# Optimization experiments

Measured on AMD Instinct MI355X. Metric: run time of the kernel, lower is better.

The kernel has to match this reference:

```python
import jax, jax.numpy as jnp
import numpy as np

B, T, E, H = 4, 2048, 1024, 16
D = E // H  # head dim = 64


def setup_inputs() -> dict:
    key = jax.random.key(0)
    k1, k2, k3 = jax.random.split(key, 3)
    g = jax.random.normal(k1, (B, T, E), dtype=jnp.float32)
    W_lift = jax.random.normal(k2, (2 * E, E), dtype=jnp.float32) * (1.0 / np.sqrt(E))
    W_proj = jax.random.normal(k3, (H, H), dtype=jnp.float32) * (1.0 / np.sqrt(H))
    return {"g": g, "W_lift": W_lift, "W_proj": W_proj}


def reference(g, W_lift, W_proj):
    b, t, e = g.shape
    h, d = H, e // H
    # lift: Linear(E, 2E, bias=False) -> split into q, k
    qk = jnp.einsum('bte,fe->btf', g, W_lift)  # (B, T, 2E)
    q, k = qk[..., :e], qk[..., e:]
    q = q.reshape(b, t, h, d).transpose(0, 2, 1, 3)  # (B, H, T, D)
    k = k.reshape(b, t, h, d).transpose(0, 2, 1, 3)  # (B, H, T, D)
    # unscaled causal scores
    a = jnp.einsum('bhqd,bhkd->bhqk', q, k)  # (B, H, T, T)
    causal = jnp.tril(jnp.ones((t, t), dtype=bool))
    a = jnp.where(causal[None, None], a, -jnp.inf)
    # masked logsumexp over key dim -> (B, H, T)
    lse = jax.scipy.special.logsumexp(a, axis=-1)
    out = lse.transpose(0, 2, 1)  # (B, T, H)
    out = jnp.einsum('bth,gh->btg', out, W_proj)  # proj Linear(H, H)
    out = out.sum(axis=2)  # (B, T)
    return out.reshape(-1, out.shape[-1])
```

## Files before the change

kernel.cpp:

```cpp
#include <hip/hip_runtime.h>
#include <hip/hip_bf16.h>

#define B_ 4
#define T_ 2048
#define E_ 1024
#define H_ 16
#define D_ 64
#define Mtot 8192
#define N2 2048
#define K_ 1024
#define PS_ (B_ * H_ * T_)
#define NKT 16
#define LOG2E 1.4426950408889634f

typedef __attribute__((ext_vector_type(8))) short short8;
typedef __attribute__((ext_vector_type(4))) float f32x4;
using bf16 = __hip_bfloat16;

__device__ __forceinline__ void async_copy16(const void* g, void* l) {
  __builtin_amdgcn_global_load_lds(
      (const __attribute__((address_space(1))) unsigned int*)g,
      (__attribute__((address_space(3))) unsigned int*)l, 16, 0, 0);
}

__global__ void cast_f32_to_bf16(const float* __restrict__ in, ushort* __restrict__ out, int n4) {
  int stride = gridDim.x * blockDim.x;
  for (int i = blockIdx.x * blockDim.x + threadIdx.x; i < n4; i += stride) {
    float4 v = reinterpret_cast<const float4*>(in)[i];
    bf16 a = __float2bfloat16(v.x), b = __float2bfloat16(v.y);
    bf16 c = __float2bfloat16(v.z), d = __float2bfloat16(v.w);
    ushort4 o = make_ushort4(*(ushort*)&a, *(ushort*)&b, *(ushort*)&c, *(ushort*)&d);
    reinterpret_cast<ushort4*>(out)[i] = o;
  }
}

#define MFMA_BF16(a, b, c) __builtin_amdgcn_mfma_f32_16x16x32_bf16(a, b, c, 0, 0, 0)

__launch_bounds__(512, 2)
__global__ void lift_gemm(const bf16* __restrict__ A, const bf16* __restrict__ Bm,
                          bf16* __restrict__ qh, bf16* __restrict__ kh) {
  __shared__ __align__(16) char sL[8][16384];
  const int bid = blockIdx.x;
  const int swz = ((bid & 7) << 5) | (bid >> 3);
  const int m0 = (swz >> 3) * 256;
  const int n0 = (swz & 7) * 256;
  const int tid = threadIdx.x;
  const int lane = tid & 63, w = tid >> 6;
  const int wm = w >> 2, wn = w & 3;
  const int lr = lane & 15, lg = lane >> 4;

  f32x4 acc[8][4];
#pragma unroll
  for (int i = 0; i < 8; ++i)
#pragma unroll
    for (int j = 0; j < 4; ++j) acc[i][j] = (f32x4)(0.0f);

  auto stage_half = [&](int slot, const bf16* gsrc, int Rbase, int kcol) {
#pragma unroll
    for (int it = 0; it < 2; ++it) {
      const int o = ((it * 512 + tid) << 4);
      const int lin = o ^ (((o >> 7) & 7) << 4);
      const int r = lin >> 7, cb = lin & 127;
      async_copy16((const char*)gsrc + ((size_t)(Rbase + r) * K_ + kcol) * 2 + cb,
                   &sL[slot][o]);
    }
  };
  auto rd = [&](int slot, int row, int khalf) -> short8 {
    int off = (row << 7) + (khalf << 6) + (lg << 4);
    off ^= (row & 7) << 4;
    return *(const short8*)&sL[slot][off];
  };

  stage_half(0, A, m0, 0);
  stage_half(1, A, m0 + 128, 0);
  stage_half(2, Bm, n0, 0);
  stage_half(3, Bm, n0 + 128, 0);

  for (int kt = 0; kt < NKT; ++kt) {
    const int cb = (kt & 1) << 2;
    const int nb = cb ^ 4;
    const int kcol = (kt + 1) * 64;
    const int aslot = cb + wm;
    const int bslot = cb + 2 + (wn >> 1);
    const int brow = (wn & 1) * 64;

    if (kt + 1 < NKT) {
      stage_half(nb + 0, A, m0, kcol);
      stage_half(nb + 1, A, m0 + 128, kcol);
      stage_half(nb + 2, Bm, n0, kcol);
      stage_half(nb + 3, Bm, n0 + 128, kcol);
      asm volatile("s_waitcnt vmcnt(8)" ::: "memory");
    } else {
      asm volatile("s_waitcnt vmcnt(0)" ::: "memory");
    }
    __builtin_amdgcn_sched_barrier(0);
    __builtin_amdgcn_s_barrier();

    short8 bf[4][2], af[4][2];
#pragma unroll
    for (int j = 0; j < 4; ++j) {
      bf[j][0] = rd(bslot, brow + j * 16 + lr, 0);
      bf[j][1] = rd(bslot, brow + j * 16 + lr, 1);
    }
#pragma unroll
    for (int i = 0; i < 4; ++i) {
      af[i][0] = rd(aslot, i * 16 + lr, 0);
      af[i][1] = rd(aslot, i * 16 + lr, 1);
    }
    __builtin_amdgcn_s_setprio(1);
#pragma unroll
    for (int i = 0; i < 4; ++i)
#pragma unroll
      for (int j = 0; j < 4; ++j) {
        acc[i][j] = MFMA_BF16(af[i][0], bf[j][0], acc[i][j]);
        acc[i][j] = MFMA_BF16(af[i][1], bf[j][1], acc[i][j]);
      }
    __builtin_amdgcn_s_setprio(0);
    short8 ah[4][2];
#pragma unroll
    for (int i = 0; i < 4; ++i) {
      ah[i][0] = rd(aslot, (i + 4) * 16 + lr, 0);
      ah[i][1] = rd(aslot, (i + 4) * 16 + lr, 1);
    }
    __builtin_amdgcn_s_setprio(1);
#pragma unroll
    for (int i = 0; i < 4; ++i)
#pragma unroll
      for (int j = 0; j < 4; ++j) {
        acc[i + 4][j] = MFMA_BF16(ah[i][0], bf[j][0], acc[i + 4][j]);
        acc[i + 4][j] = MFMA_BF16(ah[i][1], bf[j][1], acc[i + 4][j]);
      }
    __builtin_amdgcn_s_setprio(0);
    __builtin_amdgcn_sched_barrier(0);
    __builtin_amdgcn_s_barrier();
  }

  const float qscale = (n0 < E_) ? LOG2E : 1.0f;
#pragma unroll
  for (int mi = 0; mi < 8; ++mi) {
#pragma unroll
    for (int ni = 0; ni < 4; ++ni) {
#pragma unroll
      for (int r = 0; r < 4; ++r) {
        int m = m0 + wm * 128 + mi * 16 + lg * 4 + r;
        int f = n0 + wn * 64 + ni * 16 + lr;
        bf16 bv = __float2bfloat16(acc[mi][ni][r] * qscale);
        int b = m >> 11, t = m & (T_ - 1);
        int hh = (f & (E_ - 1)) >> 6, d = f & (D_ - 1);
        bf16* dst = (f < E_) ? qh : kh;
        dst[((((size_t)b * H_ + hh) * T_) + t) * D_ + d] = bv;
      }
    }
  }
}

#define LSE_QT 128

__launch_bounds__(256)
__global__ void attn_lse(const bf16* __restrict__ qh, const bf16* __restrict__ kh,
                         float* __restrict__ psum) {
  __shared__ __align__(16) char sK[2][8192];
  const int bid = blockIdx.x;
  const int qt = 15 - (bid >> 8);
  const int rem = bid & 255;
  const int bh = rem >> 2;
  const int s = rem & 3;
  const int tid = threadIdx.x;
  const int lane = tid & 63, w = tid >> 6;
  const int lr = lane & 15, lg = lane >> 4;
  const int qbase = qt * LSE_QT + w * 32;

  const bf16* qp = qh + ((size_t)bh * T_ + qbase) * D_;
  short8 qf[2][2];
#pragma unroll
  for (int f = 0; f < 2; ++f)
#pragma unroll
    for (int h = 0; h < 2; ++h)
      qf[f][h] = *(const short8*)&qp[(size_t)(f * 16 + lr) * D_ + h * 32 + lg * 8];

  float l[2][4];
#pragma unroll
  for (int f = 0; f < 2; ++f)
#pragma unroll
    for (int r = 0; r < 4; ++r) l[f][r] = 0.0f;

  const char* kbase = (const char*)(kh + (size_t)bh * T_ * D_);
  const int nfullw = qbase >> 6;
  const int maxk = 2 * qt + 1;
  const int nt = (s <= maxk) ? ((maxk - s) >> 2) + 1 : 0;

#define STAGE_K(bi, kt_)                                                      \
  do {                                                                        \
    const char* kp_ = kbase + (size_t)(kt_) * (64 * D_ * 2);                  \
    _Pragma("unroll") for (int it = 0; it < 2; ++it) {                        \
      const int o = ((w * 2 + it) << 10) | (lane << 4);                       \
      const int lin = o ^ (((o >> 7) & 7) << 4);                              \
      async_copy16(kp_ + lin, (char*)&sK[bi][0] + ((w * 2 + it) << 10));      \
    }                                                                         \
  } while (0)

  auto krd = [&](const char* kb, int row, int khalf) -> short8 {
    int off = (row << 7) + (khalf << 6) + (lg << 4);
    off ^= (row & 7) << 4;
    return *(const short8*)(kb + off);
  };

  int cur = 0;
  if (nt > 0) STAGE_K(0, s);
  for (int i = 0; i < nt; ++i) {
    if (i + 1 < nt) {
      STAGE_K(cur ^ 1, s + 4 * (i + 1));
      asm volatile("s_waitcnt vmcnt(2)" ::: "memory");
    } else {
      asm volatile("s_waitcnt vmcnt(0)" ::: "memory");
    }
    __builtin_amdgcn_sched_barrier(0);
    __builtin_amdgcn_s_barrier();

    const int kt = s + 4 * i;
    if (kt <= nfullw) {
      const char* kb = &sK[cur][0];
      short8 kf[4][2];
#pragma unroll
      for (int j = 0; j < 4; ++j) {
        kf[j][0] = krd(kb, j * 16 + lr, 0);
        kf[j][1] = krd(kb, j * 16 + lr, 1);
      }
      f32x4 sc[2][4];
#pragma unroll
      for (int f = 0; f < 2; ++f)
#pragma unroll
        for (int j = 0; j < 4; ++j) sc[f][j] = (f32x4)(0.0f);
#pragma unroll
      for (int j = 0; j < 4; ++j) {
        sc[0][j] = MFMA_BF16(qf[0][0], kf[j][0], sc[0][j]);
        sc[0][j] = MFMA_BF16(qf[0][1], kf[j][1], sc[0][j]);
        sc[1][j] = MFMA_BF16(qf[1][0], kf[j][0], sc[1][j]);
        sc[1][j] = MFMA_BF16(qf[1][1], kf[j][1], sc[1][j]);
      }
      if (kt < nfullw) {
#pragma unroll
        for (int f = 0; f < 2; ++f)
#pragma unroll
          for (int j = 0; j < 4; ++j)
#pragma unroll
            for (int r = 0; r < 4; ++r)
              l[f][r] += __builtin_amdgcn_exp2f(sc[f][j][r]);
      } else {
#pragma unroll
        for (int f = 0; f < 2; ++f)
#pragma unroll
          for (int j = 0; j < 4; ++j)
#pragma unroll
            for (int r = 0; r < 4; ++r) {
              int qrow = qbase + f * 16 + lg * 4 + r;
              int key = kt * 64 + j * 16 + lr;
              float a = (key <= qrow) ? sc[f][j][r] : -INFINITY;
              l[f][r] += __builtin_amdgcn_exp2f(a);
            }
      }
    }
    __builtin_amdgcn_sched_barrier(0);
    __builtin_amdgcn_s_barrier();
    cur ^= 1;
  }

#pragma unroll
  for (int f = 0; f < 2; ++f)
#pragma unroll
    for (int r = 0; r < 4; ++r) {
      float v = l[f][r];
      v += __shfl_xor(v, 1);
      v += __shfl_xor(v, 2);
      v += __shfl_xor(v, 4);
      v += __shfl_xor(v, 8);
      if (lr == 0)
        psum[(size_t)s * PS_ + (size_t)bh * T_ + qbase + f * 16 + lg * 4 + r] = v;
    }
}

__global__ void proj_out(const float* __restrict__ psum, const float* __restrict__ Wp,
                         float* __restrict__ out) {
  __shared__ float cw[H_];
  int tid = threadIdx.x;
  if (tid < H_) {
    float s = 0.0f;
    for (int g = 0; g < H_; ++g) s += Wp[g * H_ + tid];
    cw[tid] = s;
  }
  __syncthreads();
  int idx = blockIdx.x * blockDim.x + tid;
  int b = idx >> 11, t = idx & (T_ - 1);
  float acc = 0.0f;
#pragma unroll
  for (int h = 0; h < H_; ++h) {
    size_t base = ((size_t)(b * H_ + h) * T_) + t;
    float v = psum[base] + psum[PS_ + base] + psum[2 * (size_t)PS_ + base] +
              psum[3 * (size_t)PS_ + base];
    acc += __logf(v) * cw[h];
  }
  out[idx] = acc;
}

extern "C" void kernel_launch(void* const* d_in, const int* in_sizes, int n_in,
                              void* d_out, int out_size, void* d_ws, size_t ws_size,
                              hipStream_t stream) {
  (void)in_sizes; (void)n_in; (void)out_size; (void)ws_size;
  const float* g  = (const float*)d_in[0];
  const float* Wl = (const float*)d_in[1];
  const float* Wp = (const float*)d_in[2];
  float* out = (float*)d_out;

  char* ws = (char*)d_ws;
  size_t off = 0;
  bf16* g_bf  = (bf16*)(ws + off); off += (size_t)Mtot * K_ * 2;
  bf16* wl_bf = (bf16*)(ws + off); off += (size_t)N2 * K_ * 2;
  bf16* qh    = (bf16*)(ws + off); off += (size_t)B_ * H_ * T_ * D_ * 2;
  bf16* kh    = (bf16*)(ws + off); off += (size_t)B_ * H_ * T_ * D_ * 2;
  float* psum = (float*)(ws + off);

  cast_f32_to_bf16<<<2048, 256, 0, stream>>>(g,  (ushort*)g_bf,  (Mtot * K_) / 4);
  cast_f32_to_bf16<<<512,  256, 0, stream>>>(Wl, (ushort*)wl_bf, (N2 * K_) / 4);

  lift_gemm<<<256, 512, 0, stream>>>(g_bf, wl_bf, qh, kh);

  attn_lse<<<4096, 256, 0, stream>>>(qh, kh, psum);

  proj_out<<<(B_ * T_) / 256, 256, 0, stream>>>(psum, Wp, out);
}
```

Before: 89.25 us.

## Load GEMM B operand straight into registers with double-buffered prefetch, halving LDS

```diff
diff --git a/kernel.cpp b/kernel.cpp
--- a/kernel.cpp
+++ b/kernel.cpp
@@ -39,7 +39,7 @@
 __launch_bounds__(512, 2)
 __global__ void lift_gemm(const bf16* __restrict__ A, const bf16* __restrict__ Bm,
                           bf16* __restrict__ qh, bf16* __restrict__ kh) {
-  __shared__ __align__(16) char sL[8][16384];
+  __shared__ __align__(16) char sL[4][16384];
   const int bid = blockIdx.x;
   const int swz = ((bid & 7) << 5) | (bid >> 3);
   const int m0 = (swz >> 3) * 256;
@@ -55,13 +55,13 @@
 #pragma unroll
     for (int j = 0; j < 4; ++j) acc[i][j] = (f32x4)(0.0f);
 
-  auto stage_half = [&](int slot, const bf16* gsrc, int Rbase, int kcol) {
+  auto stage_half = [&](int slot, int Rbase, int kcol) {
 #pragma unroll
     for (int it = 0; it < 2; ++it) {
       const int o = ((it * 512 + tid) << 4);
       const int lin = o ^ (((o >> 7) & 7) << 4);
       const int r = lin >> 7, cb = lin & 127;
-      async_copy16((const char*)gsrc + ((size_t)(Rbase + r) * K_ + kcol) * 2 + cb,
+      async_copy16((const char*)A + ((size_t)(Rbase + r) * K_ + kcol) * 2 + cb,
                    &sL[slot][o]);
     }
   };
@@ -70,38 +70,40 @@
     off ^= (row & 7) << 4;
     return *(const short8*)&sL[slot][off];
   };
-
-  stage_half(0, A, m0, 0);
-  stage_half(1, A, m0 + 128, 0);
-  stage_half(2, Bm, n0, 0);
-  stage_half(3, Bm, n0 + 128, 0);
-
-  for (int kt = 0; kt < NKT; ++kt) {
-    const int cb = (kt & 1) << 2;
-    const int nb = cb ^ 4;
+  auto load_b = [&](short8 (&bf)[4][2], int kcol) {
+#pragma unroll
+    for (int j = 0; j < 4; ++j)
+#pragma unroll
+      for (int h2 = 0; h2 < 2; ++h2)
+        bf[j][h2] = *(const short8*)&Bm[(size_t)(n0 + wn * 64 + j * 16 + lr) * K_ +
+                                        kcol + h2 * 32 + lg * 8];
+  };
+
+  short8 bA[4][2], bB[4][2];
+  load_b(bA, 0);
+  stage_half(0, m0, 0);
+  stage_half(1, m0 + 128, 0);
+
+  auto kstep = [&](int kt, short8 (&bCur)[4][2], short8 (&bNext)[4][2]) {
+    const int cs = (kt & 1) << 1;
+    const int ns = cs ^ 2;
     const int kcol = (kt + 1) * 64;
-    const int aslot = cb + wm;
-    const int bslot = cb + 2 + (wn >> 1);
-    const int brow = (wn & 1) * 64;
-
-    if (kt + 1 < NKT) {
-      stage_half(nb + 0, A, m0, kcol);
-      stage_half(nb + 1, A, m0 + 128, kcol);
-      stage_half(nb + 2, Bm, n0, kcol);
-      stage_half(nb + 3, Bm, n0 + 128, kcol);
-      asm volatile("s_waitcnt vmcnt(8)" ::: "memory");
+    const bool pf = (kt + 1 < NKT);
+    const int aslot = cs + wm;
+
+    if (pf) {
+      stage_half(ns + 0, m0, kcol);
+      stage_half(ns + 1, m0 + 128, kcol);
+      asm volatile("s_waitcnt vmcnt(4)" ::: "memory");
     } else {
       asm volatile("s_waitcnt vmcnt(0)" ::: "memory");
     }
     __builtin_amdgcn_sched_barrier(0);
     __builtin_amdgcn_s_barrier();
 
-    short8 bf[4][2], af[4][2];
-#pragma unroll
-    for (int j = 0; j < 4; ++j) {
-      bf[j][0] = rd(bslot, brow + j * 16 + lr, 0);
-      bf[j][1] = rd(bslot, brow + j * 16 + lr, 1);
-    }
+    if (pf) load_b(bNext, kcol);
+
+    short8 af[4][2];
 #pragma unroll
     for (int i = 0; i < 4; ++i) {
       af[i][0] = rd(aslot, i * 16 + lr, 0);
@@ -112,8 +114,8 @@
     for (int i = 0; i < 4; ++i)
 #pragma unroll
       for (int j = 0; j < 4; ++j) {
-        acc[i][j] = MFMA_BF16(af[i][0], bf[j][0], acc[i][j]);
-        acc[i][j] = MFMA_BF16(af[i][1], bf[j][1], acc[i][j]);
+        acc[i][j] = MFMA_BF16(af[i][0], bCur[j][0], acc[i][j]);
+        acc[i][j] = MFMA_BF16(af[i][1], bCur[j][1], acc[i][j]);
       }
     __builtin_amdgcn_s_setprio(0);
     short8 ah[4][2];
@@ -127,12 +129,17 @@
     for (int i = 0; i < 4; ++i)
 #pragma unroll
       for (int j = 0; j < 4; ++j) {
-        acc[i + 4][j] = MFMA_BF16(ah[i][0], bf[j][0], acc[i + 4][j]);
-        acc[i + 4][j] = MFMA_BF16(ah[i][1], bf[j][1], acc[i + 4][j]);
+        acc[i + 4][j] = MFMA_BF16(ah[i][0], bCur[j][0], acc[i + 4][j]);
+        acc[i + 4][j] = MFMA_BF16(ah[i][1], bCur[j][1], acc[i + 4][j]);
       }
     __builtin_amdgcn_s_setprio(0);
     __builtin_amdgcn_sched_barrier(0);
     __builtin_amdgcn_s_barrier();
+  };
+
+  for (int kt2 = 0; kt2 < NKT; kt2 += 2) {
+    kstep(kt2, bA, bB);
+    kstep(kt2 + 1, bB, bA);
   }
 
   const float qscale = (n0 < E_) ? LOG2E : 1.0f;
```

After: 107.9 us. +20.9%, slower.
